# Kernel tuning notes

Hardware: AMD Instinct MI355X
Metric: run time of the kernel (lower is better)

The kernel has to match this reference:

```python
import jax, jax.numpy as jnp
import numpy as np

B, T, D = 2, 1024, 2048
E, K, H = 64, 4, 512          # n_experts, top-k, expert_dim
S, HS = 2, H * K              # shared experts, shared hidden dim
CAP = 512


def setup_inputs() -> dict:
    key = jax.random.key(0)
    ks = jax.random.split(key, 9)
    scale = 0.02
    return {
        "x": jax.random.normal(ks[0], (B, T, D), jnp.float32),
        "Wr": jax.random.normal(ks[1], (D, E), jnp.float32) * scale,
        "router_bias": jnp.zeros((E,), jnp.float32),
        "Wg": jax.random.normal(ks[2], (E, D, H), jnp.float32) * scale,
        "Wu": jax.random.normal(ks[3], (E, D, H), jnp.float32) * scale,
        "Wd": jax.random.normal(ks[4], (E, H, D), jnp.float32) * scale,
        "Sg": jax.random.normal(ks[5], (S, D, HS), jnp.float32) * scale,
        "Su": jax.random.normal(ks[6], (S, D, HS), jnp.float32) * scale,
        "Sd": jax.random.normal(ks[7], (S, HS, D), jnp.float32) * scale,
    }


def reference(x, Wr, router_bias, Wg, Wu, Wd, Sg, Su, Sd):
    Bx, Tx, Dx = x.shape
    N = Bx * Tx
    flat = x.reshape(N, Dx)                              # [N, D]

    # ---- router ----
    logits = flat @ Wr + router_bias                     # [N, E]
    scores = jax.nn.softmax(logits, axis=-1)
    topk_scores, topk_idx = jax.lax.top_k(scores, K)     # [N, K]
    topk_scores = topk_scores / topk_scores.sum(-1, keepdims=True)

    eid = topk_idx.reshape(-1)                           # [N*K] expert per assignment
    w = topk_scores.reshape(-1)                          # [N*K] combine weight
    tok = jnp.repeat(jnp.arange(N), K)                   # [N*K] source token id

    # position of each assignment within its expert's buffer
    oh = jax.nn.one_hot(eid, E, dtype=jnp.int32)         # [N*K, E]
    pos = ((jnp.cumsum(oh, axis=0) * oh).sum(-1) - 1)    # [N*K]
    valid = pos < CAP

    # ---- dispatch: scatter tokens into per-expert buffers ----
    xb = jnp.zeros((E, CAP, Dx), x.dtype).at[eid, pos].set(flat[tok], mode="drop")

    # ---- grouped SwiGLU expert FFN ----
    h = jax.nn.silu(jnp.einsum("ecd,edh->ech", xb, Wg)) * jnp.einsum("ecd,edh->ech", xb, Wu)
    yb = jnp.einsum("ech,ehd->ecd", h, Wd)               # [E, CAP, D]

    # ---- combine: gather back and weighted scatter-add to tokens ----
    y = yb[eid, jnp.minimum(pos, CAP - 1)] * (w * valid)[:, None]
    out = jnp.zeros((N, Dx), x.dtype).at[tok].add(y)

    # ---- always-on shared experts ----
    hs = jax.nn.silu(jnp.einsum("nd,sdh->nsh", flat, Sg)) * jnp.einsum("nd,sdh->nsh", flat, Su)
    out = out + jnp.einsum("nsh,shd->nd", hs, Sd)

    return out.reshape(Bx, Tx, Dx)
```

## Files before the change

### kernel.cpp

```cpp
#include <hip/hip_runtime.h>
#include <hip/hip_bf16.h>
#include <stdint.h>

#define N_TOK 2048
#define DM    2048
#define NEXP  64
#define TOPK  4
#define HEXP  512
#define CAPC  512
#define NSH   2
#define HSH   2048
#define RTB   8

typedef __attribute__((ext_vector_type(8))) short short8;
typedef __attribute__((ext_vector_type(4))) short short4v;
typedef __attribute__((ext_vector_type(4))) float f32x4;
typedef __attribute__((ext_vector_type(4))) float f4;

static __device__ __forceinline__ unsigned short f2bf(float f) {
  union { float f; unsigned u; } v; v.f = f;
  unsigned r = v.u + 0x7FFFu + ((v.u >> 16) & 1u);
  return (unsigned short)(r >> 16);
}

__global__ __launch_bounds__(256) void k_convert(const float* __restrict__ x,
                                                 unsigned short* __restrict__ xb) {
  int i = (blockIdx.x * 256 + threadIdx.x) * 8;
  f4 a = *(const f4*)(x + i);
  f4 b = *(const f4*)(x + i + 4);
  short8 o;
  o[0]=f2bf(a[0]); o[1]=f2bf(a[1]); o[2]=f2bf(a[2]); o[3]=f2bf(a[3]);
  o[4]=f2bf(b[0]); o[5]=f2bf(b[1]); o[6]=f2bf(b[2]); o[7]=f2bf(b[3]);
  *(short8*)(xb + i) = o;
}

#define ARGMAX_ROUND(S,I)                                            \
  { float bv = v; int bi = lane;                                     \
    _Pragma("unroll")                                                \
    for (int o = 32; o; o >>= 1) {                                   \
      float ov = __shfl_xor(bv, o); int oi = __shfl_xor(bi, o);      \
      if (ov > bv || (ov == bv && oi < bi)) { bv = ov; bi = oi; }    \
    }                                                                \
    S = bv; I = bi; if (lane == bi) v = -1.f; }

__global__ __launch_bounds__(256) void k_router(const float* __restrict__ x,
    const float* __restrict__ Wr, const float* __restrict__ bias,
    int* __restrict__ cnt, int* __restrict__ lists, float* __restrict__ wlist) {
  __shared__ float part[4][RTB][64];
  __shared__ float logits[RTB][64];
  int t = threadIdx.x;
  int e = t & 63, sl = t >> 6;
  int tok0 = blockIdx.x * RTB;
  const float* xp = x + (size_t)tok0 * DM;
  float acc[RTB];
#pragma unroll
  for (int i = 0; i < RTB; ++i) acc[i] = 0.f;
  for (int d = sl * 512; d < sl * 512 + 512; ++d) {
    float w = Wr[(size_t)d * NEXP + e];
#pragma unroll
    for (int i = 0; i < RTB; ++i) acc[i] += xp[(size_t)i * DM + d] * w;
  }
#pragma unroll
  for (int i = 0; i < RTB; ++i) part[sl][i][e] = acc[i];
  __syncthreads();
  for (int i = sl; i < RTB; i += 4)
    logits[i][e] = part[0][i][e] + part[1][i][e] + part[2][i][e] + part[3][i][e] + bias[e];
  __syncthreads();
  int lane = t & 63, wv = t >> 6;
  for (int i = wv * 2; i < wv * 2 + 2; ++i) {
    float lg = logits[i][lane];
    float m = lg;
#pragma unroll
    for (int o = 32; o; o >>= 1) m = fmaxf(m, __shfl_xor(m, o));
    float p = expf(lg - m);
    float sm = p;
#pragma unroll
    for (int o = 32; o; o >>= 1) sm += __shfl_xor(sm, o);
    float v = p / sm;
    float s0, s1, s2, s3; int i0, i1, i2, i3;
    ARGMAX_ROUND(s0, i0)
    ARGMAX_ROUND(s1, i1)
    ARGMAX_ROUND(s2, i2)
    ARGMAX_ROUND(s3, i3)
    float tot = s0 + s1 + s2 + s3;
    if (lane < TOPK) {
      float myw = (lane == 0 ? s0 : lane == 1 ? s1 : lane == 2 ? s2 : s3) / tot;
      int   mye = (lane == 0 ? i0 : lane == 1 ? i1 : lane == 2 ? i2 : i3);
      int pos = atomicAdd(&cnt[mye], 1);
      if (pos < CAPC) {
        lists[mye * CAPC + pos] = tok0 + i;
        wlist[mye * CAPC + pos] = myw;
      }
    }
  }
}

__global__ void k_offs(const int* __restrict__ cnt, int* __restrict__ offs) {
  int l = threadIdx.x;
  int c = min(cnt[l], CAPC);
  int sum = c;
#pragma unroll
  for (int o = 1; o < 64; o <<= 1) {
    int ov = __shfl_up(sum, o);
    if (l >= o) sum += ov;
  }
  offs[l + 1] = sum;
  if (l == 0) offs[0] = 0;
}


template<bool GATHER>
static __device__ __forceinline__ void stageA(const unsigned short* __restrict__ src,
    int lda, int m0, int Mvalid, const int* __restrict__ gl,
    unsigned short* lA, int k0) {
  int tid = threadIdx.x;
#pragma unroll
  for (int p = 0; p < 4; ++p) {
    int idx = p * 256 + tid;
    int row = idx >> 3;
    int ko  = (idx & 7) * 8;
    short8 val;
    int grow = m0 + row;
    if (grow < Mvalid) {
      int srow = GATHER ? gl[grow] : grow;
      val = *(const short8*)(src + (size_t)srow * lda + k0 + ko);
    } else {
#pragma unroll
      for (int j = 0; j < 8; ++j) val[j] = 0;
    }
    int byte = row * 128 + ko * 2;
    byte ^= (row & 7) << 4;
    *(short8*)((char*)lA + byte) = val;
  }
}

static __device__ __forceinline__ void stageB(const float* __restrict__ B, int ldb,
    int k0, int n0, unsigned short* lB) {
  int tid = threadIdx.x;
  int kb = tid >> 4;
  int nb = tid & 15;
  const float* p = B + (size_t)(k0 + kb * 4) * ldb + n0 + nb * 4;
  f4 r0 = *(const f4*)(p);
  f4 r1 = *(const f4*)(p + ldb);
  f4 r2 = *(const f4*)(p + 2 * (size_t)ldb);
  f4 r3 = *(const f4*)(p + 3 * (size_t)ldb);
#pragma unroll
  for (int c = 0; c < 4; ++c) {
    short4v vv;
    vv[0] = (short)f2bf(r0[c]); vv[1] = (short)f2bf(r1[c]);
    vv[2] = (short)f2bf(r2[c]); vv[3] = (short)f2bf(r3[c]);
    int n = nb * 4 + c;
    int byte = n * 128 + kb * 8;
    byte ^= (n & 7) << 4;
    *(short4v*)((char*)lB + byte) = vv;
  }
}

static __device__ __forceinline__ short8 frag_ld(const unsigned short* lds, int row, int kElem) {
  int byte = row * 128 + kElem * 2;
  byte ^= (row & 7) << 4;
  return *(const short8*)((const char*)lds + byte);
}

static __device__ __forceinline__ void mma1(const unsigned short* lA, const unsigned short* lB,
    f32x4 (&acc)[4][2], int wm, int wn, int lane) {
  int r16 = lane & 15;
  int kg  = (lane >> 4) * 8;
#pragma unroll
  for (int kk = 0; kk < 2; ++kk) {
    int kb = kk * 32 + kg;
    short8 a[4], b[2];
#pragma unroll
    for (int mf = 0; mf < 4; ++mf) a[mf] = frag_ld(lA, wm + mf * 16 + r16, kb);
#pragma unroll
    for (int nf = 0; nf < 2; ++nf) b[nf] = frag_ld(lB, wn + nf * 16 + r16, kb);
#pragma unroll
    for (int mf = 0; mf < 4; ++mf)
#pragma unroll
      for (int nf = 0; nf < 2; ++nf)
        acc[mf][nf] = __builtin_amdgcn_mfma_f32_16x16x32_bf16(a[mf], b[nf], acc[mf][nf], 0, 0, 0);
  }
}

static __device__ __forceinline__ void mma2(const unsigned short* lA,
    const unsigned short* lBg, const unsigned short* lBu,
    f32x4 (&accg)[4][2], f32x4 (&accu)[4][2], int wm, int wn, int lane) {
  int r16 = lane & 15;
  int kg  = (lane >> 4) * 8;
#pragma unroll
  for (int kk = 0; kk < 2; ++kk) {
    int kb = kk * 32 + kg;
    short8 a[4], bg[2], bu[2];
#pragma unroll
    for (int mf = 0; mf < 4; ++mf) a[mf] = frag_ld(lA, wm + mf * 16 + r16, kb);
#pragma unroll
    for (int nf = 0; nf < 2; ++nf) {
      bg[nf] = frag_ld(lBg, wn + nf * 16 + r16, kb);
      bu[nf] = frag_ld(lBu, wn + nf * 16 + r16, kb);
    }
#pragma unroll
    for (int mf = 0; mf < 4; ++mf)
#pragma unroll
      for (int nf = 0; nf < 2; ++nf) {
        accg[mf][nf] = __builtin_amdgcn_mfma_f32_16x16x32_bf16(a[mf], bg[nf], accg[mf][nf], 0, 0, 0);
        accu[mf][nf] = __builtin_amdgcn_mfma_f32_16x16x32_bf16(a[mf], bu[nf], accu[mf][nf], 0, 0, 0);
      }
  }
}

static __device__ __forceinline__ float silu_mul(float g, float u) {
  return g / (1.f + expf(-g)) * u;
}

__global__ __launch_bounds__(256) void k_expert_gateup(const unsigned short* __restrict__ xbf,
    const float* __restrict__ Wg, const float* __restrict__ Wu,
    const int* __restrict__ cnt, const int* __restrict__ offs,
    const int* __restrict__ lists, unsigned short* __restrict__ hws) {
  int e = blockIdx.y;
  int ne = min(cnt[e], CAPC);
  if (ne == 0) return;
  int n0 = blockIdx.x * 64;
  const float* Bg = Wg + (size_t)e * DM * HEXP;
  const float* Bu = Wu + (size_t)e * DM * HEXP;
  const int* lst = lists + e * CAPC;
  int base = offs[e];
  __shared__ unsigned short lA[128 * 64];
  __shared__ unsigned short lBg[64 * 64];
  __shared__ unsigned short lBu[64 * 64];
  int lane = threadIdx.x & 63, wv = threadIdx.x >> 6;
  int wm = (wv >> 1) * 64, wn = (wv & 1) * 32;
  for (int m0 = 0; m0 < ne; m0 += 128) {
    f32x4 accg[4][2] = {};
    f32x4 accu[4][2] = {};
    for (int k0 = 0; k0 < DM; k0 += 64) {
      stageA<true>(xbf, DM, m0, ne, lst, lA, k0);
      stageB(Bg, HEXP, k0, n0, lBg);
      stageB(Bu, HEXP, k0, n0, lBu);
      __syncthreads();
      mma2(lA, lBg, lBu, accg, accu, wm, wn, lane);
      __syncthreads();
    }
#pragma unroll
    for (int mf = 0; mf < 4; ++mf)
#pragma unroll
      for (int r = 0; r < 4; ++r) {
        int rl = m0 + wm + mf * 16 + (lane >> 4) * 4 + r;
        if (rl < ne) {
#pragma unroll
          for (int nf = 0; nf < 2; ++nf) {
            int col = n0 + wn + nf * 16 + (lane & 15);
            float h = silu_mul(accg[mf][nf][r], accu[mf][nf][r]);
            hws[(size_t)(base + rl) * HEXP + col] = f2bf(h);
          }
        }
      }
  }
}

__global__ __launch_bounds__(256) void k_shared_gateup(const unsigned short* __restrict__ xbf,
    const float* __restrict__ Sg, const float* __restrict__ Su,
    unsigned short* __restrict__ hs) {
  int n0 = blockIdx.x * 64;
  int m0 = blockIdx.y * 128;
  int s  = blockIdx.z;
  const float* Bg = Sg + (size_t)s * DM * HSH;
  const float* Bu = Su + (size_t)s * DM * HSH;
  __shared__ unsigned short lA[128 * 64];
  __shared__ unsigned short lBg[64 * 64];
  __shared__ unsigned short lBu[64 * 64];
  int lane = threadIdx.x & 63, wv = threadIdx.x >> 6;
  int wm = (wv >> 1) * 64, wn = (wv & 1) * 32;
  f32x4 accg[4][2] = {};
  f32x4 accu[4][2] = {};
  for (int k0 = 0; k0 < DM; k0 += 64) {
    stageA<false>(xbf, DM, m0, N_TOK, nullptr, lA, k0);
    stageB(Bg, HSH, k0, n0, lBg);
    stageB(Bu, HSH, k0, n0, lBu);
    __syncthreads();
    mma2(lA, lBg, lBu, accg, accu, wm, wn, lane);
    __syncthreads();
  }
#pragma unroll
  for (int mf = 0; mf < 4; ++mf)
#pragma unroll
    for (int nf = 0; nf < 2; ++nf)
#pragma unroll
      for (int r = 0; r < 4; ++r) {
        int row = m0 + wm + mf * 16 + (lane >> 4) * 4 + r;
        int col = n0 + wn + nf * 16 + (lane & 15);
        float h = silu_mul(accg[mf][nf][r], accu[mf][nf][r]);
        hs[(size_t)row * (NSH * HSH) + s * HSH + col] = f2bf(h);
      }
}

__global__ __launch_bounds__(256) void k_shared_down(const unsigned short* __restrict__ hs,
    const float* __restrict__ Sd, float* __restrict__ out) {
  int n0 = blockIdx.x * 64;
  int m0 = blockIdx.y * 128;
  __shared__ unsigned short lA[128 * 64];
  __shared__ unsigned short lB[64 * 64];
  int lane = threadIdx.x & 63, wv = threadIdx.x >> 6;
  int wm = (wv >> 1) * 64, wn = (wv & 1) * 32;
  f32x4 acc[4][2] = {};
  for (int k0 = 0; k0 < NSH * HSH; k0 += 64) {
    stageA<false>(hs, NSH * HSH, m0, N_TOK, nullptr, lA, k0);
    stageB(Sd, DM, k0, n0, lB);
    __syncthreads();
    mma1(lA, lB, acc, wm, wn, lane);
    __syncthreads();
  }
#pragma unroll
  for (int mf = 0; mf < 4; ++mf)
#pragma unroll
    for (int nf = 0; nf < 2; ++nf)
#pragma unroll
      for (int r = 0; r < 4; ++r) {
        int row = m0 + wm + mf * 16 + (lane >> 4) * 4 + r;
        int col = n0 + wn + nf * 16 + (lane & 15);
        out[(size_t)row * DM + col] = acc[mf][nf][r];
      }
}

__global__ __launch_bounds__(256) void k_expert_down(const unsigned short* __restrict__ hws,
    const float* __restrict__ Wd, const int* __restrict__ cnt, const int* __restrict__ offs,
    const int* __restrict__ lists, const float* __restrict__ wlist,
    float* __restrict__ out) {
  int e = blockIdx.y;
  int ne = min(cnt[e], CAPC);
  if (ne == 0) return;
  int n0 = blockIdx.x * 64;
  const float* B = Wd + (size_t)e * HEXP * DM;
  const unsigned short* A = hws + (size_t)offs[e] * HEXP;
  __shared__ unsigned short lA[128 * 64];
  __shared__ unsigned short lB[64 * 64];
  int lane = threadIdx.x & 63, wv = threadIdx.x >> 6;
  int wm = (wv >> 1) * 64, wn = (wv & 1) * 32;
  for (int m0 = 0; m0 < ne; m0 += 128) {
    f32x4 acc[4][2] = {};
    for (int k0 = 0; k0 < HEXP; k0 += 64) {
      stageA<false>(A, HEXP, m0, ne, nullptr, lA, k0);
      stageB(B, DM, k0, n0, lB);
      __syncthreads();
      mma1(lA, lB, acc, wm, wn, lane);
      __syncthreads();
    }
#pragma unroll
    for (int mf = 0; mf < 4; ++mf)
#pragma unroll
      for (int r = 0; r < 4; ++r) {
        int rl = m0 + wm + mf * 16 + (lane >> 4) * 4 + r;
        if (rl < ne) {
          int tok  = lists[e * CAPC + rl];
          float w  = wlist[e * CAPC + rl];
#pragma unroll
          for (int nf = 0; nf < 2; ++nf) {
            int col = n0 + wn + nf * 16 + (lane & 15);
            atomicAdd(out + (size_t)tok * DM + col, acc[mf][nf][r] * w);
          }
        }
      }
  }
}

extern "C" void kernel_launch(void* const* d_in, const int* in_sizes, int n_in,
                              void* d_out, int out_size, void* d_ws, size_t ws_size,
                              hipStream_t stream) {
  const float* x    = (const float*)d_in[0];
  const float* Wr   = (const float*)d_in[1];
  const float* bias = (const float*)d_in[2];
  const float* Wg   = (const float*)d_in[3];
  const float* Wu   = (const float*)d_in[4];
  const float* Wd   = (const float*)d_in[5];
  const float* Sg   = (const float*)d_in[6];
  const float* Su   = (const float*)d_in[7];
  const float* Sd   = (const float*)d_in[8];
  float* out = (float*)d_out;
  char* ws = (char*)d_ws;

  const size_t off_cnt   = 0;
  const size_t off_offs  = 256;
  const size_t off_lists = 1024;
  const size_t off_wlist = off_lists + (size_t)NEXP * CAPC * 4;
  const size_t off_xbf   = off_wlist + (size_t)NEXP * CAPC * 4;
  const size_t off_hs    = off_xbf + (size_t)N_TOK * DM * 2;
  const size_t off_h     = off_hs + (size_t)N_TOK * NSH * HSH * 2;
  const size_t req       = off_h + (size_t)N_TOK * TOPK * HEXP * 2;
  if (ws_size < req) return;

  int* cnt            = (int*)(ws + off_cnt);
  int* offs           = (int*)(ws + off_offs);
  int* lists          = (int*)(ws + off_lists);
  float* wlist        = (float*)(ws + off_wlist);
  unsigned short* xbf = (unsigned short*)(ws + off_xbf);
  unsigned short* hs  = (unsigned short*)(ws + off_hs);
  unsigned short* hws = (unsigned short*)(ws + off_h);

  hipMemsetAsync(cnt, 0, NEXP * sizeof(int), stream);
  k_convert<<<(N_TOK * DM) / (256 * 8), 256, 0, stream>>>(x, xbf);
  k_router<<<N_TOK / RTB, 256, 0, stream>>>(x, Wr, bias, cnt, lists, wlist);
  k_offs<<<1, 64, 0, stream>>>(cnt, offs);
  k_expert_gateup<<<dim3(HEXP / 64, NEXP), 256, 0, stream>>>(xbf, Wg, Wu, cnt, offs, lists, hws);
  k_shared_gateup<<<dim3(HSH / 64, N_TOK / 128, NSH), 256, 0, stream>>>(xbf, Sg, Su, hs);
  k_shared_down<<<dim3(DM / 64, N_TOK / 128), 256, 0, stream>>>(hs, Sd, out);
  k_expert_down<<<dim3(DM / 64, NEXP), 256, 0, stream>>>(hws, Wd, cnt, offs, lists, wlist, out);
}
```

Measured before the change: 791.6 us.

## Prefetch next K-tile into registers to overlap global loads with MFMA

Splits the LDS staging routines into separate global-load and LDS-write steps. In all four GEMM kernels, the next K-tile of A and B is loaded into registers while the current tile is computed, so global-memory latency overlaps with the matrix math. The cost is higher register pressure from the extra prefetch registers, which may reduce occupancy.

```diff
diff --git a/kernel.cpp b/kernel.cpp
--- a/kernel.cpp
+++ b/kernel.cpp
@@ -110,45 +110,57 @@
 
 
 template<bool GATHER>
-static __device__ __forceinline__ void stageA(const unsigned short* __restrict__ src,
-    int lda, int m0, int Mvalid, const int* __restrict__ gl,
-    unsigned short* lA, int k0) {
+static __device__ __forceinline__ void loadA(const unsigned short* __restrict__ src,
+    int lda, int m0, int Mvalid, const int* __restrict__ gl, int k0, short8 (&r)[4]) {
   int tid = threadIdx.x;
 #pragma unroll
   for (int p = 0; p < 4; ++p) {
     int idx = p * 256 + tid;
     int row = idx >> 3;
     int ko  = (idx & 7) * 8;
-    short8 val;
     int grow = m0 + row;
     if (grow < Mvalid) {
       int srow = GATHER ? gl[grow] : grow;
-      val = *(const short8*)(src + (size_t)srow * lda + k0 + ko);
+      r[p] = *(const short8*)(src + (size_t)srow * lda + k0 + ko);
     } else {
 #pragma unroll
-      for (int j = 0; j < 8; ++j) val[j] = 0;
-    }
+      for (int j = 0; j < 8; ++j) r[p][j] = 0;
+    }
+  }
+}
+
+static __device__ __forceinline__ void writeA(const short8 (&r)[4], unsigned short* lA) {
+  int tid = threadIdx.x;
+#pragma unroll
+  for (int p = 0; p < 4; ++p) {
+    int idx = p * 256 + tid;
+    int row = idx >> 3;
+    int ko  = (idx & 7) * 8;
     int byte = row * 128 + ko * 2;
     byte ^= (row & 7) << 4;
-    *(short8*)((char*)lA + byte) = val;
-  }
-}
-
-static __device__ __forceinline__ void stageB(const float* __restrict__ B, int ldb,
-    int k0, int n0, unsigned short* lB) {
+    *(short8*)((char*)lA + byte) = r[p];
+  }
+}
+
+static __device__ __forceinline__ void loadB(const float* __restrict__ B, int ldb,
+    int k0, int n0, f4 (&r)[4]) {
   int tid = threadIdx.x;
   int kb = tid >> 4;
   int nb = tid & 15;
   const float* p = B + (size_t)(k0 + kb * 4) * ldb + n0 + nb * 4;
-  f4 r0 = *(const f4*)(p);
-  f4 r1 = *(const f4*)(p + ldb);
-  f4 r2 = *(const f4*)(p + 2 * (size_t)ldb);
-  f4 r3 = *(const f4*)(p + 3 * (size_t)ldb);
+#pragma unroll
+  for (int q = 0; q < 4; ++q) r[q] = *(const f4*)(p + (size_t)q * ldb);
+}
+
+static __device__ __forceinline__ void writeB(const f4 (&r)[4], unsigned short* lB) {
+  int tid = threadIdx.x;
+  int kb = tid >> 4;
+  int nb = tid & 15;
 #pragma unroll
   for (int c = 0; c < 4; ++c) {
     short4v vv;
-    vv[0] = (short)f2bf(r0[c]); vv[1] = (short)f2bf(r1[c]);
-    vv[2] = (short)f2bf(r2[c]); vv[3] = (short)f2bf(r3[c]);
+    vv[0] = (short)f2bf(r[0][c]); vv[1] = (short)f2bf(r[1][c]);
+    vv[2] = (short)f2bf(r[2][c]); vv[3] = (short)f2bf(r[3][c]);
     int n = nb * 4 + c;
     int byte = n * 128 + kb * 8;
     byte ^= (n & 7) << 4;
@@ -232,10 +244,20 @@
   for (int m0 = 0; m0 < ne; m0 += 128) {
     f32x4 accg[4][2] = {};
     f32x4 accu[4][2] = {};
+    short8 ra[4]; f4 rg[4], ru[4];
+    loadA<true>(xbf, DM, m0, ne, lst, 0, ra);
+    loadB(Bg, HEXP, 0, n0, rg);
+    loadB(Bu, HEXP, 0, n0, ru);
     for (int k0 = 0; k0 < DM; k0 += 64) {
-      stageA<true>(xbf, DM, m0, ne, lst, lA, k0);
-      stageB(Bg, HEXP, k0, n0, lBg);
-      stageB(Bu, HEXP, k0, n0, lBu);
+      writeA(ra, lA);
+      writeB(rg, lBg);
+      writeB(ru, lBu);
+      int kn = k0 + 64;
+      if (kn < DM) {
+        loadA<true>(xbf, DM, m0, ne, lst, kn, ra);
+        loadB(Bg, HEXP, kn, n0, rg);
+        loadB(Bu, HEXP, kn, n0, ru);
+      }
       __syncthreads();
       mma2(lA, lBg, lBu, accg, accu, wm, wn, lane);
       __syncthreads();
@@ -272,10 +294,20 @@
   int wm = (wv >> 1) * 64, wn = (wv & 1) * 32;
   f32x4 accg[4][2] = {};
   f32x4 accu[4][2] = {};
+  short8 ra[4]; f4 rg[4], ru[4];
+  loadA<false>(xbf, DM, m0, N_TOK, nullptr, 0, ra);
+  loadB(Bg, HSH, 0, n0, rg);
+  loadB(Bu, HSH, 0, n0, ru);
   for (int k0 = 0; k0 < DM; k0 += 64) {
-    stageA<false>(xbf, DM, m0, N_TOK, nullptr, lA, k0);
-    stageB(Bg, HSH, k0, n0, lBg);
-    stageB(Bu, HSH, k0, n0, lBu);
+    writeA(ra, lA);
+    writeB(rg, lBg);
+    writeB(ru, lBu);
+    int kn = k0 + 64;
+    if (kn < DM) {
+      loadA<false>(xbf, DM, m0, N_TOK, nullptr, kn, ra);
+      loadB(Bg, HSH, kn, n0, rg);
+      loadB(Bu, HSH, kn, n0, ru);
+    }
     __syncthreads();
     mma2(lA, lBg, lBu, accg, accu, wm, wn, lane);
     __syncthreads();
@@ -302,9 +334,17 @@
   int lane = threadIdx.x & 63, wv = threadIdx.x >> 6;
   int wm = (wv >> 1) * 64, wn = (wv & 1) * 32;
   f32x4 acc[4][2] = {};
+  short8 ra[4]; f4 rb[4];
+  loadA<false>(hs, NSH * HSH, m0, N_TOK, nullptr, 0, ra);
+  loadB(Sd, DM, 0, n0, rb);
   for (int k0 = 0; k0 < NSH * HSH; k0 += 64) {
-    stageA<false>(hs, NSH * HSH, m0, N_TOK, nullptr, lA, k0);
-    stageB(Sd, DM, k0, n0, lB);
+    writeA(ra, lA);
+    writeB(rb, lB);
+    int kn = k0 + 64;
+    if (kn < NSH * HSH) {
+      loadA<false>(hs, NSH * HSH, m0, N_TOK, nullptr, kn, ra);
+      loadB(Sd, DM, kn, n0, rb);
+    }
     __syncthreads();
     mma1(lA, lB, acc, wm, wn, lane);
     __syncthreads();
@@ -337,9 +377,17 @@
   int wm = (wv >> 1) * 64, wn = (wv & 1) * 32;
   for (int m0 = 0; m0 < ne; m0 += 128) {
     f32x4 acc[4][2] = {};
+    short8 ra[4]; f4 rb[4];
+    loadA<false>(A, HEXP, m0, ne, nullptr, 0, ra);
+    loadB(B, DM, 0, n0, rb);
     for (int k0 = 0; k0 < HEXP; k0 += 64) {
-      stageA<false>(A, HEXP, m0, ne, nullptr, lA, k0);
-      stageB(B, DM, k0, n0, lB);
+      writeA(ra, lA);
+      writeB(rb, lB);
+      int kn = k0 + 64;
+      if (kn < HEXP) {
+        loadA<false>(A, HEXP, m0, ne, nullptr, kn, ra);
+        loadB(B, DM, kn, n0, rb);
+      }
       __syncthreads();
       mma1(lA, lB, acc, wm, wn, lane);
       __syncthreads();
```

After: 669.4 us. 15.4% less time.

## Stage GEMM tiles via direct global-to-LDS loads and convert weights at fragment load

Applied to the files above, without the earlier changes.

Replaces the register-staged A/B tile loads in all four GEMM kernels with global_load_lds 16-byte direct-to-LDS transfers. Weights are now kept as fp32 in LDS and converted to bf16 when building MFMA fragments, and the A-tile swizzle is applied on the global source address. Out-of-range rows are clamped instead of zero-filled, and launch bounds now request 3 blocks per CU. This removes VGPR round-trips and conversion work from the staging path. The cost is doubled LDS footprint for B, strided scalar fp32 LDS reads with repeated conversion per fragment (likely bank conflicts), and no double-buffering.

```diff
diff --git a/kernel.cpp b/kernel.cpp
--- a/kernel.cpp
+++ b/kernel.cpp
@@ -13,9 +13,12 @@
 #define RTB   8
 
 typedef __attribute__((ext_vector_type(8))) short short8;
-typedef __attribute__((ext_vector_type(4))) short short4v;
 typedef __attribute__((ext_vector_type(4))) float f32x4;
 typedef __attribute__((ext_vector_type(4))) float f4;
+
+#define GLDS16(g, l) __builtin_amdgcn_global_load_lds(                     \
+    (const __attribute__((address_space(1))) void*)(g),                    \
+    (__attribute__((address_space(3))) void*)(l), 16, 0, 0)
 
 static __device__ __forceinline__ unsigned short f2bf(float f) {
   union { float f; unsigned u; } v; v.f = f;
@@ -109,60 +112,20 @@
 }
 
 
-template<bool GATHER>
-static __device__ __forceinline__ void stageA(const unsigned short* __restrict__ src,
-    int lda, int m0, int Mvalid, const int* __restrict__ gl,
-    unsigned short* lA, int k0) {
-  int tid = threadIdx.x;
-#pragma unroll
-  for (int p = 0; p < 4; ++p) {
-    int idx = p * 256 + tid;
-    int row = idx >> 3;
-    int ko  = (idx & 7) * 8;
-    short8 val;
-    int grow = m0 + row;
-    if (grow < Mvalid) {
-      int srow = GATHER ? gl[grow] : grow;
-      val = *(const short8*)(src + (size_t)srow * lda + k0 + ko);
-    } else {
-#pragma unroll
-      for (int j = 0; j < 8; ++j) val[j] = 0;
-    }
-    int byte = row * 128 + ko * 2;
-    byte ^= (row & 7) << 4;
-    *(short8*)((char*)lA + byte) = val;
-  }
-}
-
-static __device__ __forceinline__ void stageB(const float* __restrict__ B, int ldb,
-    int k0, int n0, unsigned short* lB) {
-  int tid = threadIdx.x;
-  int kb = tid >> 4;
-  int nb = tid & 15;
-  const float* p = B + (size_t)(k0 + kb * 4) * ldb + n0 + nb * 4;
-  f4 r0 = *(const f4*)(p);
-  f4 r1 = *(const f4*)(p + ldb);
-  f4 r2 = *(const f4*)(p + 2 * (size_t)ldb);
-  f4 r3 = *(const f4*)(p + 3 * (size_t)ldb);
-#pragma unroll
-  for (int c = 0; c < 4; ++c) {
-    short4v vv;
-    vv[0] = (short)f2bf(r0[c]); vv[1] = (short)f2bf(r1[c]);
-    vv[2] = (short)f2bf(r2[c]); vv[3] = (short)f2bf(r3[c]);
-    int n = nb * 4 + c;
-    int byte = n * 128 + kb * 8;
-    byte ^= (n & 7) << 4;
-    *(short4v*)((char*)lB + byte) = vv;
-  }
-}
-
-static __device__ __forceinline__ short8 frag_ld(const unsigned short* lds, int row, int kElem) {
+static __device__ __forceinline__ short8 frag_ldA(const unsigned short* lds, int row, int kElem) {
   int byte = row * 128 + kElem * 2;
   byte ^= (row & 7) << 4;
   return *(const short8*)((const char*)lds + byte);
 }
 
-static __device__ __forceinline__ void mma1(const unsigned short* lA, const unsigned short* lB,
+static __device__ __forceinline__ short8 bfragB(const float* lB, int nl, int kb) {
+  short8 r;
+#pragma unroll
+  for (int j = 0; j < 8; ++j) r[j] = (short)f2bf(lB[(kb + j) * 64 + nl]);
+  return r;
+}
+
+static __device__ __forceinline__ void mma1f(const unsigned short* lA, const float* lB,
     f32x4 (&acc)[4][2], int wm, int wn, int lane) {
   int r16 = lane & 15;
   int kg  = (lane >> 4) * 8;
@@ -171,9 +134,9 @@
     int kb = kk * 32 + kg;
     short8 a[4], b[2];
 #pragma unroll
-    for (int mf = 0; mf < 4; ++mf) a[mf] = frag_ld(lA, wm + mf * 16 + r16, kb);
-#pragma unroll
-    for (int nf = 0; nf < 2; ++nf) b[nf] = frag_ld(lB, wn + nf * 16 + r16, kb);
+    for (int mf = 0; mf < 4; ++mf) a[mf] = frag_ldA(lA, wm + mf * 16 + r16, kb);
+#pragma unroll
+    for (int nf = 0; nf < 2; ++nf) b[nf] = bfragB(lB, wn + nf * 16 + r16, kb);
 #pragma unroll
     for (int mf = 0; mf < 4; ++mf)
 #pragma unroll
@@ -182,8 +145,8 @@
   }
 }
 
-static __device__ __forceinline__ void mma2(const unsigned short* lA,
-    const unsigned short* lBg, const unsigned short* lBu,
+static __device__ __forceinline__ void mma2f(const unsigned short* lA,
+    const float* lBg, const float* lBu,
     f32x4 (&accg)[4][2], f32x4 (&accu)[4][2], int wm, int wn, int lane) {
   int r16 = lane & 15;
   int kg  = (lane >> 4) * 8;
@@ -192,11 +155,11 @@
     int kb = kk * 32 + kg;
     short8 a[4], bg[2], bu[2];
 #pragma unroll
-    for (int mf = 0; mf < 4; ++mf) a[mf] = frag_ld(lA, wm + mf * 16 + r16, kb);
+    for (int mf = 0; mf < 4; ++mf) a[mf] = frag_ldA(lA, wm + mf * 16 + r16, kb);
 #pragma unroll
     for (int nf = 0; nf < 2; ++nf) {
-      bg[nf] = frag_ld(lBg, wn + nf * 16 + r16, kb);
-      bu[nf] = frag_ld(lBu, wn + nf * 16 + r16, kb);
+      bg[nf] = bfragB(lBg, wn + nf * 16 + r16, kb);
+      bu[nf] = bfragB(lBu, wn + nf * 16 + r16, kb);
     }
 #pragma unroll
     for (int mf = 0; mf < 4; ++mf)
@@ -212,7 +175,36 @@
   return g / (1.f + expf(-g)) * u;
 }
 
-__global__ __launch_bounds__(256) void k_expert_gateup(const unsigned short* __restrict__ xbf,
+#define A_SETUP(asrc, SROW_EXPR)                                            \
+  const unsigned short* asrc[4];                                            \
+  {                                                                         \
+    _Pragma("unroll")                                                       \
+    for (int p = 0; p < 4; ++p) {                                           \
+      int row = wv * 32 + p * 8 + (lane >> 3);                              \
+      int srow = (SROW_EXPR);                                               \
+      asrc[p] = Abase + (size_t)srow * lda + (((lane & 7) ^ (row & 7)) << 3);\
+    }                                                                       \
+  }
+
+#define B_SETUP(bsrc, Bbase, ldb)                                           \
+  const float* bsrc[4];                                                     \
+  {                                                                         \
+    _Pragma("unroll")                                                       \
+    for (int p = 0; p < 4; ++p) {                                           \
+      int k = wv * 16 + p * 4 + (lane >> 4);                                \
+      bsrc[p] = (Bbase) + (size_t)k * (ldb) + n0 + (lane & 15) * 4;         \
+    }                                                                       \
+  }
+
+#define A_STAGE(asrc, lA, k0)                                               \
+  _Pragma("unroll")                                                         \
+  for (int p = 0; p < 4; ++p) GLDS16(asrc[p] + (k0), (lA) + wv * 2048 + p * 512);
+
+#define B_STAGE(bsrc, lB, k0, ldb)                                          \
+  _Pragma("unroll")                                                         \
+  for (int p = 0; p < 4; ++p) GLDS16(bsrc[p] + (size_t)(k0) * (ldb), (lB) + wv * 1024 + p * 256);
+
+__global__ __launch_bounds__(256, 3) void k_expert_gateup(const unsigned short* __restrict__ xbf,
     const float* __restrict__ Wg, const float* __restrict__ Wu,
     const int* __restrict__ cnt, const int* __restrict__ offs,
     const int* __restrict__ lists, unsigned short* __restrict__ hws) {
@@ -225,19 +217,24 @@
   const int* lst = lists + e * CAPC;
   int base = offs[e];
   __shared__ unsigned short lA[128 * 64];
-  __shared__ unsigned short lBg[64 * 64];
-  __shared__ unsigned short lBu[64 * 64];
-  int lane = threadIdx.x & 63, wv = threadIdx.x >> 6;
+  __shared__ float lBg[64 * 64];
+  __shared__ float lBu[64 * 64];
+  int tid = threadIdx.x;
+  int lane = tid & 63, wv = tid >> 6;
   int wm = (wv >> 1) * 64, wn = (wv & 1) * 32;
+  const unsigned short* Abase = xbf; const int lda = DM;
+  B_SETUP(bgsrc, Bg, HEXP)
+  B_SETUP(busrc, Bu, HEXP)
   for (int m0 = 0; m0 < ne; m0 += 128) {
+    A_SETUP(asrc, lst[min(m0 + row, ne - 1)])
     f32x4 accg[4][2] = {};
     f32x4 accu[4][2] = {};
     for (int k0 = 0; k0 < DM; k0 += 64) {
-      stageA<true>(xbf, DM, m0, ne, lst, lA, k0);
-      stageB(Bg, HEXP, k0, n0, lBg);
-      stageB(Bu, HEXP, k0, n0, lBu);
+      A_STAGE(asrc, lA, k0)
+      B_STAGE(bgsrc, lBg, k0, HEXP)
+      B_STAGE(busrc, lBu, k0, HEXP)
       __syncthreads();
-      mma2(lA, lBg, lBu, accg, accu, wm, wn, lane);
+      mma2f(lA, lBg, lBu, accg, accu, wm, wn, lane);
       __syncthreads();
     }
 #pragma unroll
@@ -257,7 +254,7 @@
   }
 }
 
-__global__ __launch_bounds__(256) void k_shared_gateup(const unsigned short* __restrict__ xbf,
+__global__ __launch_bounds__(256, 3) void k_shared_gateup(const unsigned short* __restrict__ xbf,
     const float* __restrict__ Sg, const float* __restrict__ Su,
     unsigned short* __restrict__ hs) {
   int n0 = blockIdx.x * 64;
@@ -266,18 +263,23 @@
   const float* Bg = Sg + (size_t)s * DM * HSH;
   const float* Bu = Su + (size_t)s * DM * HSH;
   __shared__ unsigned short lA[128 * 64];
-  __shared__ unsigned short lBg[64 * 64];
-  __shared__ unsigned short lBu[64 * 64];
-  int lane = threadIdx.x & 63, wv = threadIdx.x >> 6;
+  __shared__ float lBg[64 * 64];
+  __shared__ float lBu[64 * 64];
+  int tid = threadIdx.x;
+  int lane = tid & 63, wv = tid >> 6;
   int wm = (wv >> 1) * 64, wn = (wv & 1) * 32;
+  const unsigned short* Abase = xbf; const int lda = DM;
+  B_SETUP(bgsrc, Bg, HSH)
+  B_SETUP(busrc, Bu, HSH)
+  A_SETUP(asrc, m0 + row)
   f32x4 accg[4][2] = {};
   f32x4 accu[4][2] = {};
   for (int k0 = 0; k0 < DM; k0 += 64) {
-    stageA<false>(xbf, DM, m0, N_TOK, nullptr, lA, k0);
-    stageB(Bg, HSH, k0, n0, lBg);
-    stageB(Bu, HSH, k0, n0, lBu);
+    A_STAGE(asrc, lA, k0)
+    B_STAGE(bgsrc, lBg, k0, HSH)
+    B_STAGE(busrc, lBu, k0, HSH)
     __syncthreads();
-    mma2(lA, lBg, lBu, accg, accu, wm, wn, lane);
+    mma2f(lA, lBg, lBu, accg, accu, wm, wn, lane);
     __syncthreads();
   }
 #pragma unroll
@@ -293,20 +295,24 @@
       }
 }
 
-__global__ __launch_bounds__(256) void k_shared_down(const unsigned short* __restrict__ hs,
+__global__ __launch_bounds__(256, 3) void k_shared_down(const unsigned short* __restrict__ hs,
     const float* __restrict__ Sd, float* __restrict__ out) {
   int n0 = blockIdx.x * 64;
   int m0 = blockIdx.y * 128;
   __shared__ unsigned short lA[128 * 64];
-  __shared__ unsigned short lB[64 * 64];
-  int lane = threadIdx.x & 63, wv = threadIdx.x >> 6;
+  __shared__ float lB[64 * 64];
+  int tid = threadIdx.x;
+  int lane = tid & 63, wv = tid >> 6;
   int wm = (wv >> 1) * 64, wn = (wv & 1) * 32;
+  const unsigned short* Abase = hs; const int lda = NSH * HSH;
+  B_SETUP(bsrc, Sd, DM)
+  A_SETUP(asrc, m0 + row)
   f32x4 acc[4][2] = {};
   for (int k0 = 0; k0 < NSH * HSH; k0 += 64) {
-    stageA<false>(hs, NSH * HSH, m0, N_TOK, nullptr, lA, k0);
-    stageB(Sd, DM, k0, n0, lB);
+    A_STAGE(asrc, lA, k0)
+    B_STAGE(bsrc, lB, k0, DM)
     __syncthreads();
-    mma1(lA, lB, acc, wm, wn, lane);
+    mma1f(lA, lB, acc, wm, wn, lane);
     __syncthreads();
   }
 #pragma unroll
@@ -321,7 +327,7 @@
       }
 }
 
-__global__ __launch_bounds__(256) void k_expert_down(const unsigned short* __restrict__ hws,
+__global__ __launch_bounds__(256, 3) void k_expert_down(const unsigned short* __restrict__ hws,
     const float* __restrict__ Wd, const int* __restrict__ cnt, const int* __restrict__ offs,
     const int* __restrict__ lists, const float* __restrict__ wlist,
     float* __restrict__ out) {
@@ -330,18 +336,21 @@
   if (ne == 0) return;
   int n0 = blockIdx.x * 64;
   const float* B = Wd + (size_t)e * HEXP * DM;
-  const unsigned short* A = hws + (size_t)offs[e] * HEXP;
   __shared__ unsigned short lA[128 * 64];
-  __shared__ unsigned short lB[64 * 64];
-  int lane = threadIdx.x & 63, wv = threadIdx.x >> 6;
+  __shared__ float lB[64 * 64];
+  int tid = threadIdx.x;
+  int lane = tid & 63, wv = tid >> 6;
   int wm = (wv >> 1) * 64, wn = (wv & 1) * 32;
+  const unsigned short* Abase = hws + (size_t)offs[e] * HEXP; const int lda = HEXP;
+  B_SETUP(bsrc, B, DM)
   for (int m0 = 0; m0 < ne; m0 += 128) {
+    A_SETUP(asrc, min(m0 + row, ne - 1))
     f32x4 acc[4][2] = {};
     for (int k0 = 0; k0 < HEXP; k0 += 64) {
-      stageA<false>(A, HEXP, m0, ne, nullptr, lA, k0);
-      stageB(B, DM, k0, n0, lB);
+      A_STAGE(asrc, lA, k0)
+      B_STAGE(bsrc, lB, k0, DM)
       __syncthreads();
-      mma1(lA, lB, acc, wm, wn, lane);
+      mma1f(lA, lB, acc, wm, wn, lane);
       __syncthreads();
     }
 #pragma unroll
```

Measured after the change: 670.9 us. -15.3%, faster.
